# Kernel optimization log

Hardware: AMD Instinct MI355X
Metric: run time of the kernel (lower is better)

The kernel has to match this reference:

```python
import jax, jax.numpy as jnp
import numpy as np

HIDDEN = 1024
HEADS = 16
HEAD_DIM = HIDDEN // HEADS


def setup_inputs() -> dict:
    key = jax.random.key(0)
    ks = jax.random.split(key, 11)
    B, S = 2, 2048
    s = 1.0 / np.sqrt(HIDDEN)
    return {
        "query": jax.random.normal(ks[0], (B, S, HIDDEN), jnp.float32),
        "key": jax.random.normal(ks[1], (B, S, HIDDEN), jnp.float32),
        "value": jax.random.normal(ks[2], (B, S, HIDDEN), jnp.float32),
        "Wq": jax.random.uniform(ks[3], (HIDDEN, HIDDEN), jnp.float32, -s, s),
        "bq": jax.random.uniform(ks[4], (HIDDEN,), jnp.float32, -s, s),
        "Wk": jax.random.uniform(ks[5], (HIDDEN, HIDDEN), jnp.float32, -s, s),
        "bk": jax.random.uniform(ks[6], (HIDDEN,), jnp.float32, -s, s),
        "Wv": jax.random.uniform(ks[7], (HIDDEN, HIDDEN), jnp.float32, -s, s),
        "bv": jax.random.uniform(ks[8], (HIDDEN,), jnp.float32, -s, s),
        "Wo": jax.random.uniform(ks[9], (HIDDEN, HIDDEN), jnp.float32, -s, s),
        "bo": jax.random.uniform(ks[10], (HIDDEN,), jnp.float32, -s, s),
    }


def reference(query, key, value, Wq, bq, Wk, bk, Wv, bv, Wo, bo):
    B, Sq, _ = query.shape
    Sk = key.shape[1]
    # projections (torch Linear: x @ W^T + b)
    Q = (query @ Wq.T + bq).reshape(B, Sq, HEADS, HEAD_DIM).transpose(0, 2, 1, 3)
    K = (key @ Wk.T + bk).reshape(B, Sk, HEADS, HEAD_DIM).transpose(0, 2, 1, 3)
    V = (value @ Wv.T + bv).reshape(B, Sk, HEADS, HEAD_DIM).transpose(0, 2, 1, 3)
    scale = jnp.sqrt(jnp.float32(HEAD_DIM))
    scores = jnp.einsum("bhqd,bhkd->bhqk", Q, K) / scale  # [B,H,Sq,Sk]
    # causal mask (is_causal=True, Sq>1)
    causal = jnp.tril(jnp.ones((Sq, Sk), dtype=bool))
    scores = jnp.where(causal[None, None], scores, -jnp.inf)
    attn = jax.nn.softmax(scores, axis=-1)
    out = jnp.einsum("bhqk,bhkd->bhqd", attn, V)
    out = out.transpose(0, 2, 1, 3).reshape(B, Sq, HIDDEN)
    return out @ Wo.T + bo
```

## Files before the change

kernel.cpp:

```cpp
#include <hip/hip_runtime.h>
#include <hip/hip_bf16.h>


typedef __attribute__((ext_vector_type(4))) float f32x4;
typedef __attribute__((ext_vector_type(8))) short bf16x8;
typedef unsigned short u16;

#define SEQ   2048
#define NH    16
#define HD    64
#define HID   1024
#define CEXP  0.1803368801f
#define MEG   1048576u

#define BAR()  __builtin_amdgcn_s_barrier()
#define SCHED0() __builtin_amdgcn_sched_barrier(0)

static __device__ __forceinline__ u16 f2bf(float f) {
  union { __hip_bfloat16 h; u16 u; } c;
  c.h = __float2bfloat16(f);
  return c.u;
}

static __device__ __forceinline__ int swz(int row, int col8) {
  return col8 ^ ((row & 7) << 3);
}

static __device__ __forceinline__ void gll16(const void* g, void* l) {
  __builtin_amdgcn_global_load_lds(
      (const __attribute__((address_space(1))) void*)g,
      (__attribute__((address_space(3))) void*)l, 16, 0, 0);
}

__global__ __launch_bounds__(256) void cvt_kernel(
    const float* __restrict__ Wq, const float* __restrict__ Wk,
    const float* __restrict__ Wv, const float* __restrict__ Wo,
    const float* __restrict__ q, const float* __restrict__ k,
    const float* __restrict__ v,
    u16* __restrict__ wsout, u16* __restrict__ dob) {
  const int y = blockIdx.y;
  const int c = y & 3;
  const float* src;
  u16* dst;
  if (y < 4) {
    src = (y == 0) ? Wq : (y == 1) ? Wk : (y == 2) ? Wv : Wo;
    dst = wsout + (size_t)y * MEG;
  } else if (y < 8) {
    src = q + (size_t)c * MEG;
    dst = wsout + 4u * MEG + (size_t)c * MEG;
  } else if (y < 12) {
    src = k + (size_t)c * MEG;
    dst = dob + (size_t)c * MEG;
  } else {
    src = v + (size_t)c * MEG;
    dst = dob + 4u * MEG + (size_t)c * MEG;
  }
  int i = (blockIdx.x * 256 + threadIdx.x) * 4;
  float4 f = *(const float4*)(src + i);
  ushort4 o;
  o.x = f2bf(f.x); o.y = f2bf(f.y); o.z = f2bf(f.z); o.w = f2bf(f.w);
  *(ushort4*)(dst + i) = o;
}

__global__ __launch_bounds__(256) void proj_kernel(
    const u16* __restrict__ Xq, const u16* __restrict__ Xk,
    const u16* __restrict__ Xv, const u16* __restrict__ Wc,
    const float* __restrict__ bq, const float* __restrict__ bk,
    const float* __restrict__ bvp,
    u16* __restrict__ Qo, u16* __restrict__ Ko, u16* __restrict__ Vto) {
  __shared__ u16 As[2][128 * 64];
  __shared__ u16 Bs[2][128 * 64];

  const int tid  = threadIdx.x;
  const int lane = tid & 63;
  const int wid  = tid >> 6;
  const int wm   = wid >> 1, wn = wid & 1;
  const int l15  = lane & 15;
  const int lhi  = lane >> 4;
  const int z    = blockIdx.z;
  const int bm   = blockIdx.x * 128;
  const int bn   = blockIdx.y * 128;

  const u16* X = (z == 0) ? Xq : (z == 1) ? Xk : Xv;
  const u16* W = Wc + (size_t)z * (HID * HID);
  const float* bias = (z == 0) ? bq : (z == 1) ? bk : bvp;

  f32x4 acc[4][4];
#pragma unroll
  for (int i = 0; i < 4; i++)
#pragma unroll
    for (int j = 0; j < 4; j++) acc[i][j] = (f32x4){0.f, 0.f, 0.f, 0.f};

  const int lrow  = lane >> 3;
  const int gcol8 = lane & 7;

#define PROJ_STAGE(buf, k0)                                                       \
  {                                                                               \
    _Pragma("unroll")                                                             \
    for (int c = 0; c < 4; c++) {                                                 \
      const int row  = c * 32 + wid * 8 + lrow;                                   \
      const int scol = (gcol8 ^ (row & 7)) * 8;      \
      gll16(X + (size_t)(bm + row) * HID + (k0) + scol,                           \
            (char*)&As[buf][0] + c * 4096 + wid * 1024);                          \
      gll16(W + (size_t)(bn + row) * HID + (k0) + scol,                           \
            (char*)&Bs[buf][0] + c * 4096 + wid * 1024);                          \
    }                                                                             \
  }

  PROJ_STAGE(0, 0);
  for (int t = 0; t < 16; t++) {
    BAR();
    if (t < 15) {
      PROJ_STAGE((t + 1) & 1, (t + 1) * 64);
      asm volatile("s_waitcnt vmcnt(8)" ::: "memory");
    } else {
      asm volatile("s_waitcnt vmcnt(0)" ::: "memory");
    }
    BAR();
    SCHED0();
    const u16* A = &As[t & 1][0];
    const u16* B = &Bs[t & 1][0];
#pragma unroll
    for (int ks = 0; ks < 2; ks++) {
      bf16x8 af[4], bfm[4];
#pragma unroll
      for (int i = 0; i < 4; i++) {
        const int row = wm * 64 + i * 16 + l15;
        af[i] = *(const bf16x8*)&A[row * 64 + swz(row, ks * 32 + lhi * 8)];
      }
#pragma unroll
      for (int j = 0; j < 4; j++) {
        const int row = wn * 64 + j * 16 + l15;
        bfm[j] = *(const bf16x8*)&B[row * 64 + swz(row, ks * 32 + lhi * 8)];
      }
#pragma unroll
      for (int i = 0; i < 4; i++)
#pragma unroll
        for (int j = 0; j < 4; j++)
          acc[i][j] = __builtin_amdgcn_mfma_f32_16x16x32_bf16(af[i], bfm[j], acc[i][j], 0, 0, 0);
    }
  }
#undef PROJ_STAGE

  const int bb = bm >> 11;
#pragma unroll
  for (int j = 0; j < 4; j++) {
    const int n = bn + wn * 64 + j * 16 + l15;
    const float bv_ = bias[n];
    const int h = n >> 6, d = n & 63;
    if (z == 2) {
#pragma unroll
      for (int i = 0; i < 4; i++) {
        const int s0 = (bm + wm * 64 + i * 16 + lhi * 4) & 2047;
        ushort4 t;
        t.x = f2bf(acc[i][j][0] + bv_);
        t.y = f2bf(acc[i][j][1] + bv_);
        t.z = f2bf(acc[i][j][2] + bv_);
        t.w = f2bf(acc[i][j][3] + bv_);
        *(ushort4*)&Vto[((size_t)(bb * NH + h) * HD + d) * SEQ + s0] = t;
      }
    } else {
      u16* O = z ? Ko : Qo;
#pragma unroll
      for (int i = 0; i < 4; i++)
#pragma unroll
        for (int r = 0; r < 4; r++) {
          const int m = bm + wm * 64 + i * 16 + lhi * 4 + r;
          const int s = m & 2047;
          O[(((size_t)(bb * NH + h) * SEQ + s) << 6) + d] = f2bf(acc[i][j][r] + bv_);
        }
    }
  }
}

__global__ __launch_bounds__(512) void attn_kernel(
    const u16* __restrict__ Q, const u16* __restrict__ K,
    const u16* __restrict__ Vt, u16* __restrict__ Aout) {
  __shared__ __align__(16) char pool[34816];

  const int tid  = threadIdx.x;
  const int lane = tid & 63;
  const int wid  = tid >> 6;
  const int l15  = lane & 15;
  const int lhi  = lane >> 4;

  const int flat = blockIdx.x;
  const int slot = flat >> 3;
  const int bh   = (flat & 7) * 4 + (slot & 3);
  const int qt   = 15 - (slot >> 2);
  const int b    = bh >> 4, h = bh & 15;
  const size_t base = (size_t)bh * SEQ * HD;

  u16* Ksh = (u16*)(pool);
  u16* Vsh = (u16*)(pool + 8192);
  u16* Psh = (u16*)(pool + 16384 + wid * 2304);

  const int qrow = qt * 128 + wid * 16 + l15;
  bf16x8 aq[2];
  aq[0] = *(const bf16x8*)&Q[base + (size_t)qrow * HD + lhi * 8];
  aq[1] = *(const bf16x8*)&Q[base + (size_t)qrow * HD + 32 + lhi * 8];

  f32x4 o[4];
#pragma unroll
  for (int n = 0; n < 4; n++) o[n] = (f32x4){0.f, 0.f, 0.f, 0.f};
  float m_s = -1e30f, l_s = 0.f;

  const int srow = tid >> 3;
  const int sd   = (tid & 7) * 8;

  bf16x8 pk, pv;

#define ATTN_LOAD(kt_)                                                            \
  {                                                                               \
    pk = *(const bf16x8*)&K[base + (size_t)((kt_) * 64 + srow) * HD + sd];        \
    pv = *(const bf16x8*)&Vt[base + (size_t)srow * SEQ + (kt_) * 64 + sd];        \
  }

  ATTN_LOAD(0);

  const int nkt = 2 * qt + 2;
  for (int kt = 0; kt < nkt; ++kt) {
    BAR();
    *(bf16x8*)&Ksh[srow * 64 + swz(srow, sd)] = pk;
    *(bf16x8*)&Vsh[srow * 64 + swz(srow, sd)] = pv;
    if (kt + 1 < nkt) ATTN_LOAD(kt + 1);
    asm volatile("s_waitcnt lgkmcnt(0)" ::: "memory");
    BAR();
    SCHED0();
    {
      f32x4 sc[4];
      __builtin_amdgcn_s_setprio(1);
#pragma unroll
      for (int n = 0; n < 4; n++) {
        sc[n] = (f32x4){0.f, 0.f, 0.f, 0.f};
#pragma unroll
        for (int ks = 0; ks < 2; ks++) {
          const int krow = n * 16 + l15;
          bf16x8 bk = *(const bf16x8*)&Ksh[krow * 64 + swz(krow, ks * 32 + lhi * 8)];
          sc[n] = __builtin_amdgcn_mfma_f32_16x16x32_bf16(bk, aq[ks], sc[n], 0, 0, 0);
        }
      }
      __builtin_amdgcn_s_setprio(0);
      if (kt >= 2 * qt) {
#pragma unroll
        for (int n = 0; n < 4; n++)
#pragma unroll
          for (int r = 0; r < 4; r++)
            if (kt * 64 + n * 16 + lhi * 4 + r > qrow) sc[n][r] = -1e30f;
      }
      float mx = -1e30f;
#pragma unroll
      for (int n = 0; n < 4; n++)
        mx = fmaxf(mx, fmaxf(fmaxf(sc[n][0], sc[n][1]), fmaxf(sc[n][2], sc[n][3])));
      mx = fmaxf(mx, __shfl_xor(mx, 16, 64));
      mx = fmaxf(mx, __shfl_xor(mx, 32, 64));
      if (__any(mx > m_s + 64.0f)) {
        const float mnew = fmaxf(m_s, mx);
        const float fac = __builtin_amdgcn_exp2f((m_s - mnew) * CEXP);
        l_s *= fac;
        m_s = mnew;
        float facr[4];
#pragma unroll
        for (int r = 0; r < 4; r++) facr[r] = __shfl(fac, lhi * 4 + r, 64);
#pragma unroll
        for (int n = 0; n < 4; n++) {
          o[n][0] *= facr[0]; o[n][1] *= facr[1];
          o[n][2] *= facr[2]; o[n][3] *= facr[3];
        }
      }
      const float nmc = -m_s * CEXP;
      float ps = 0.f;
      u16 pb[4][4];
#pragma unroll
      for (int n = 0; n < 4; n++)
#pragma unroll
        for (int r = 0; r < 4; r++) {
          const float e = __builtin_amdgcn_exp2f(fmaf(sc[n][r], CEXP, nmc));
          ps += e;
          pb[n][r] = f2bf(e);
        }
      ps += __shfl_xor(ps, 16, 64);
      ps += __shfl_xor(ps, 32, 64);
      l_s += ps;
#pragma unroll
      for (int n = 0; n < 4; n++) {
        ushort4 t; t.x = pb[n][0]; t.y = pb[n][1]; t.z = pb[n][2]; t.w = pb[n][3];
        *(ushort4*)&Psh[l15 * 72 + n * 16 + lhi * 4] = t;
      }
      bf16x8 ap0 = *(const bf16x8*)&Psh[l15 * 72 + lhi * 8];
      bf16x8 ap1 = *(const bf16x8*)&Psh[l15 * 72 + 32 + lhi * 8];
      __builtin_amdgcn_s_setprio(1);
#pragma unroll
      for (int n = 0; n < 4; n++) {
        const int vrow = n * 16 + l15;
        bf16x8 bv0 = *(const bf16x8*)&Vsh[vrow * 64 + swz(vrow, lhi * 8)];
        bf16x8 bv1 = *(const bf16x8*)&Vsh[vrow * 64 + swz(vrow, 32 + lhi * 8)];
        o[n] = __builtin_amdgcn_mfma_f32_16x16x32_bf16(ap0, bv0, o[n], 0, 0, 0);
        o[n] = __builtin_amdgcn_mfma_f32_16x16x32_bf16(ap1, bv1, o[n], 0, 0, 0);
      }
      __builtin_amdgcn_s_setprio(0);
    }
  }
#undef ATTN_LOAD

  float l_o[4];
#pragma unroll
  for (int r = 0; r < 4; r++) l_o[r] = __shfl(l_s, lhi * 4 + r, 64);
#pragma unroll
  for (int n = 0; n < 4; n++) {
#pragma unroll
    for (int r = 0; r < 4; r++) {
      const int rowg = qt * 128 + wid * 16 + lhi * 4 + r;
      Aout[(((size_t)(b * SEQ + rowg)) << 10) + h * 64 + n * 16 + l15] =
          f2bf(o[n][r] / l_o[r]);
    }
  }
}

__global__ __launch_bounds__(256) void oproj_kernel(
    const u16* __restrict__ X, const u16* __restrict__ W,
    const float* __restrict__ bias, float* __restrict__ Out) {
  __shared__ u16 As[2][128 * 64];
  __shared__ u16 Bs[2][64 * 64];

  const int tid  = threadIdx.x;
  const int lane = tid & 63;
  const int wid  = tid >> 6;
  const int wm   = wid >> 1, wn = wid & 1;
  const int l15  = lane & 15;
  const int lhi  = lane >> 4;
  const int bm   = blockIdx.x * 128;
  const int bn   = blockIdx.y * 64;

  f32x4 acc[4][2];
#pragma unroll
  for (int i = 0; i < 4; i++)
#pragma unroll
    for (int j = 0; j < 2; j++) acc[i][j] = (f32x4){0.f, 0.f, 0.f, 0.f};

  const int lrow  = lane >> 3;
  const int gcol8 = lane & 7;

#define OPROJ_STAGE(buf, k0)                                                      \
  {                                                                               \
    _Pragma("unroll")                                                             \
    for (int c = 0; c < 4; c++) {                                                 \
      const int row  = c * 32 + wid * 8 + lrow;                                   \
      const int scol = (gcol8 ^ (row & 7)) * 8;                                   \
      gll16(X + (size_t)(bm + row) * HID + (k0) + scol,                           \
            (char*)&As[buf][0] + c * 4096 + wid * 1024);                          \
      if (c < 2)                                                                  \
        gll16(W + (size_t)(bn + row) * HID + (k0) + scol,                         \
              (char*)&Bs[buf][0] + c * 4096 + wid * 1024);                        \
    }                                                                             \
  }

  OPROJ_STAGE(0, 0);
  for (int t = 0; t < 16; t++) {
    BAR();
    if (t < 15) {
      OPROJ_STAGE((t + 1) & 1, (t + 1) * 64);
      asm volatile("s_waitcnt vmcnt(6)" ::: "memory");
    } else {
      asm volatile("s_waitcnt vmcnt(0)" ::: "memory");
    }
    BAR();
    SCHED0();
    const u16* A = &As[t & 1][0];
    const u16* B = &Bs[t & 1][0];
#pragma unroll
    for (int ks = 0; ks < 2; ks++) {
      bf16x8 af[4], bfm[2];
#pragma unroll
      for (int i = 0; i < 4; i++) {
        const int row = wm * 64 + i * 16 + l15;
        af[i] = *(const bf16x8*)&A[row * 64 + swz(row, ks * 32 + lhi * 8)];
      }
#pragma unroll
      for (int j = 0; j < 2; j++) {
        const int row = wn * 32 + j * 16 + l15;
        bfm[j] = *(const bf16x8*)&B[row * 64 + swz(row, ks * 32 + lhi * 8)];
      }
#pragma unroll
      for (int i = 0; i < 4; i++)
#pragma unroll
        for (int j = 0; j < 2; j++)
          acc[i][j] = __builtin_amdgcn_mfma_f32_16x16x32_bf16(af[i], bfm[j], acc[i][j], 0, 0, 0);
    }
  }
#undef OPROJ_STAGE

#pragma unroll
  for (int j = 0; j < 2; j++) {
    const int n = bn + wn * 32 + j * 16 + l15;
    const float bv_ = bias[n];
#pragma unroll
    for (int i = 0; i < 4; i++)
#pragma unroll
      for (int r = 0; r < 4; r++) {
        const int m = bm + wm * 64 + i * 16 + lhi * 4 + r;
        Out[(size_t)m * HID + n] = acc[i][j][r] + bv_;
      }
  }
}

extern "C" void kernel_launch(void* const* d_in, const int* in_sizes, int n_in,
                              void* d_out, int out_size, void* d_ws, size_t ws_size,
                              hipStream_t stream) {
  const float* q  = (const float*)d_in[0];
  const float* k  = (const float*)d_in[1];
  const float* v  = (const float*)d_in[2];
  const float* Wq = (const float*)d_in[3];
  const float* bq = (const float*)d_in[4];
  const float* Wk = (const float*)d_in[5];
  const float* bk = (const float*)d_in[6];
  const float* Wv = (const float*)d_in[7];
  const float* bv = (const float*)d_in[8];
  const float* Wo = (const float*)d_in[9];
  const float* bo = (const float*)d_in[10];

  u16* ws   = (u16*)d_ws;
  u16* wqkv = ws;
  u16* wob  = ws + 3u * MEG;
  u16* qb   = ws + 4u * MEG;
  u16* Qb   = ws + 8u * MEG;
  u16* Kb   = ws + 12u * MEG;
  u16* Vtb  = ws + 16u * MEG;
  u16* Ab   = qb;
  u16* kbf  = (u16*)d_out;
  u16* vbf  = (u16*)d_out + 4u * MEG;

  cvt_kernel<<<dim3(1024, 16), 256, 0, stream>>>(Wq, Wk, Wv, Wo, q, k, v, ws, kbf);

  proj_kernel<<<dim3(32, 8, 3), 256, 0, stream>>>(qb, kbf, vbf, wqkv, bq, bk, bv,
                                                  Qb, Kb, Vtb);

  attn_kernel<<<dim3(512), 512, 0, stream>>>(Qb, Kb, Vtb, Ab);

  oproj_kernel<<<dim3(32, 16), 256, 0, stream>>>(Ab, wob, bo, (float*)d_out);
}
```

Before: 115.3 us.

## Double-buffer K/V in LDS and compute next QK^T ahead of softmax

The attention loop now double-buffers K and V tiles in shared memory and software-pipelines the QK^T MFMA of the next key tile before the softmax and PV of the current tile. The aim is to let matrix-core work overlap the exp and reduction phase and to hide LDS-write and barrier latency. In exchange, shared memory grows from about 34 KB to 51 KB per block and an extra set of score registers is kept live, which may reduce occupancy or add register pressure.

```diff
diff --git a/kernel.cpp b/kernel.cpp
--- a/kernel.cpp
+++ b/kernel.cpp
@@ -176,7 +176,7 @@
 __global__ __launch_bounds__(512) void attn_kernel(
     const u16* __restrict__ Q, const u16* __restrict__ K,
     const u16* __restrict__ Vt, u16* __restrict__ Aout) {
-  __shared__ __align__(16) char pool[34816];
+  __shared__ __align__(16) char pool[51200];
 
   const int tid  = threadIdx.x;
   const int lane = tid & 63;
@@ -191,9 +191,7 @@
   const int b    = bh >> 4, h = bh & 15;
   const size_t base = (size_t)bh * SEQ * HD;
 
-  u16* Ksh = (u16*)(pool);
-  u16* Vsh = (u16*)(pool + 8192);
-  u16* Psh = (u16*)(pool + 16384 + wid * 2304);
+  u16* Psh = (u16*)(pool + 32768 + wid * 2304);
 
   const int qrow = qt * 128 + wid * 16 + l15;
   bf16x8 aq[2];
@@ -207,51 +205,71 @@
 
   const int srow = tid >> 3;
   const int sd   = (tid & 7) * 8;
+  const int swoff = srow * 64 + swz(srow, sd);
 
   bf16x8 pk, pv;
 
-#define ATTN_LOAD(kt_)                                                            \
+#define LOADR(kt_)                                                                \
   {                                                                               \
     pk = *(const bf16x8*)&K[base + (size_t)((kt_) * 64 + srow) * HD + sd];        \
     pv = *(const bf16x8*)&Vt[base + (size_t)srow * SEQ + (kt_) * 64 + sd];        \
   }
-
-  ATTN_LOAD(0);
+#define WRITE_LDS(b_)                                                             \
+  {                                                                               \
+    *(bf16x8*)&((u16*)(pool + (b_) * 8192))[swoff] = pk;                          \
+    *(bf16x8*)&((u16*)(pool + 16384 + (b_) * 8192))[swoff] = pv;                  \
+  }
+#define QKT(dst, b_, kt_)                                                         \
+  {                                                                               \
+    const u16* Ksh_ = (const u16*)(pool + (b_) * 8192);                           \
+    __builtin_amdgcn_s_setprio(1);                                                \
+    _Pragma("unroll")                                                             \
+    for (int n = 0; n < 4; n++) {                                                 \
+      dst[n] = (f32x4){0.f, 0.f, 0.f, 0.f};                                       \
+      _Pragma("unroll")                                                           \
+      for (int ks = 0; ks < 2; ks++) {                                            \
+        const int krow = n * 16 + l15;                                            \
+        bf16x8 bk = *(const bf16x8*)&Ksh_[krow * 64 + swz(krow, ks * 32 + lhi * 8)]; \
+        dst[n] = __builtin_amdgcn_mfma_f32_16x16x32_bf16(bk, aq[ks], dst[n], 0, 0, 0); \
+      }                                                                           \
+    }                                                                             \
+    __builtin_amdgcn_s_setprio(0);                                                \
+    if ((kt_) >= 2 * qt) {                                                        \
+      _Pragma("unroll")                                                           \
+      for (int n = 0; n < 4; n++)                                                 \
+        _Pragma("unroll")                                                         \
+        for (int r = 0; r < 4; r++)                                               \
+          if ((kt_) * 64 + n * 16 + lhi * 4 + r > qrow) dst[n][r] = -1e30f;       \
+    }                                                                             \
+  }
 
   const int nkt = 2 * qt + 2;
+
+  LOADR(0);
+  WRITE_LDS(0);
+  if (nkt > 1) LOADR(1);
+  asm volatile("s_waitcnt lgkmcnt(0)" ::: "memory");
+  BAR();
+  SCHED0();
+  f32x4 scc[4], scn[4];
+  QKT(scc, 0, 0);
+
   for (int kt = 0; kt < nkt; ++kt) {
-    BAR();
-    *(bf16x8*)&Ksh[srow * 64 + swz(srow, sd)] = pk;
-    *(bf16x8*)&Vsh[srow * 64 + swz(srow, sd)] = pv;
-    if (kt + 1 < nkt) ATTN_LOAD(kt + 1);
-    asm volatile("s_waitcnt lgkmcnt(0)" ::: "memory");
-    BAR();
-    SCHED0();
+    const int nk = kt + 1;
+    if (nk < nkt) {
+      BAR();
+      WRITE_LDS(nk & 1);
+      if (nk + 1 < nkt) LOADR(nk + 1);
+      asm volatile("s_waitcnt lgkmcnt(0)" ::: "memory");
+      BAR();
+      SCHED0();
+      QKT(scn, nk & 1, nk);
+    }
     {
-      f32x4 sc[4];
-      __builtin_amdgcn_s_setprio(1);
-#pragma unroll
-      for (int n = 0; n < 4; n++) {
-        sc[n] = (f32x4){0.f, 0.f, 0.f, 0.f};
-#pragma unroll
-        for (int ks = 0; ks < 2; ks++) {
-          const int krow = n * 16 + l15;
-          bf16x8 bk = *(const bf16x8*)&Ksh[krow * 64 + swz(krow, ks * 32 + lhi * 8)];
-          sc[n] = __builtin_amdgcn_mfma_f32_16x16x32_bf16(bk, aq[ks], sc[n], 0, 0, 0);
-        }
-      }
-      __builtin_amdgcn_s_setprio(0);
-      if (kt >= 2 * qt) {
-#pragma unroll
-        for (int n = 0; n < 4; n++)
-#pragma unroll
-          for (int r = 0; r < 4; r++)
-            if (kt * 64 + n * 16 + lhi * 4 + r > qrow) sc[n][r] = -1e30f;
-      }
       float mx = -1e30f;
 #pragma unroll
       for (int n = 0; n < 4; n++)
-        mx = fmaxf(mx, fmaxf(fmaxf(sc[n][0], sc[n][1]), fmaxf(sc[n][2], sc[n][3])));
+        mx = fmaxf(mx, fmaxf(fmaxf(scc[n][0], scc[n][1]), fmaxf(scc[n][2], scc[n][3])));
       mx = fmaxf(mx, __shfl_xor(mx, 16, 64));
       mx = fmaxf(mx, __shfl_xor(mx, 32, 64));
       if (__any(mx > m_s + 64.0f)) {
@@ -275,7 +293,7 @@
       for (int n = 0; n < 4; n++)
 #pragma unroll
         for (int r = 0; r < 4; r++) {
-          const float e = __builtin_amdgcn_exp2f(fmaf(sc[n][r], CEXP, nmc));
+          const float e = __builtin_amdgcn_exp2f(fmaf(scc[n][r], CEXP, nmc));
           ps += e;
           pb[n][r] = f2bf(e);
         }
@@ -289,6 +307,7 @@
       }
       bf16x8 ap0 = *(const bf16x8*)&Psh[l15 * 72 + lhi * 8];
       bf16x8 ap1 = *(const bf16x8*)&Psh[l15 * 72 + 32 + lhi * 8];
+      const u16* Vsh = (const u16*)(pool + 16384 + (kt & 1) * 8192);
       __builtin_amdgcn_s_setprio(1);
 #pragma unroll
       for (int n = 0; n < 4; n++) {
@@ -300,8 +319,12 @@
       }
       __builtin_amdgcn_s_setprio(0);
     }
-  }
-#undef ATTN_LOAD
+#pragma unroll
+    for (int n = 0; n < 4; n++) scc[n] = scn[n];
+  }
+#undef LOADR
+#undef WRITE_LDS
+#undef QKT
 
   float l_o[4];
 #pragma unroll
```

After: 115.8 us. No clear change (+0.4%).

## Rewrite attention kernel with 32x32x16 MFMA and register-resident P

Applied to the files above, without the earlier changes.

The attention kernel moves from 16x16x32 to 32x32x16 bf16 MFMA tiles. Each of 4 waves now owns 32 query rows, so blocks shrink to 256 threads with a launch bound of 4 blocks per CU. The K and V tiles use new swizzled LDS layouts matched to the 32x32 operand pattern. Because the score accumulator layout matches the A-operand layout, the softmax probabilities are packed to bf16 in registers and fed directly to the PV MFMA, removing the per-wave P round trip through LDS. The cost is higher register pressure from the f32x16 accumulators and fewer waves per block to hide latency.

```diff
diff --git a/kernel.cpp b/kernel.cpp
--- a/kernel.cpp
+++ b/kernel.cpp
@@ -2,8 +2,9 @@
 #include <hip/hip_bf16.h>
 
 
-typedef __attribute__((ext_vector_type(4))) float f32x4;
-typedef __attribute__((ext_vector_type(8))) short bf16x8;
+typedef __attribute__((ext_vector_type(4)))  float f32x4;
+typedef __attribute__((ext_vector_type(16))) float f32x16;
+typedef __attribute__((ext_vector_type(8)))  short bf16x8;
 typedef unsigned short u16;
 
 #define SEQ   2048
@@ -13,7 +14,7 @@
 #define CEXP  0.1803368801f
 #define MEG   1048576u
 
-#define BAR()  __builtin_amdgcn_s_barrier()
+#define BAR()    __builtin_amdgcn_s_barrier()
 #define SCHED0() __builtin_amdgcn_sched_barrier(0)
 
 static __device__ __forceinline__ u16 f2bf(float f) {
@@ -99,7 +100,7 @@
     _Pragma("unroll")                                                             \
     for (int c = 0; c < 4; c++) {                                                 \
       const int row  = c * 32 + wid * 8 + lrow;                                   \
-      const int scol = (gcol8 ^ (row & 7)) * 8;      \
+      const int scol = (gcol8 ^ (row & 7)) * 8;                                   \
       gll16(X + (size_t)(bm + row) * HID + (k0) + scol,                           \
             (char*)&As[buf][0] + c * 4096 + wid * 1024);                          \
       gll16(W + (size_t)(bn + row) * HID + (k0) + scol,                           \
@@ -173,16 +174,18 @@
   }
 }
 
-__global__ __launch_bounds__(512) void attn_kernel(
+__global__ __launch_bounds__(256, 4) void attn_kernel(
     const u16* __restrict__ Q, const u16* __restrict__ K,
     const u16* __restrict__ Vt, u16* __restrict__ Aout) {
-  __shared__ __align__(16) char pool[34816];
+  __shared__ __align__(16) char pool[16384];
+  u16* Ksh = (u16*)pool;
+  u16* Vsh = (u16*)(pool + 8192);
 
   const int tid  = threadIdx.x;
   const int lane = tid & 63;
   const int wid  = tid >> 6;
-  const int l15  = lane & 15;
-  const int lhi  = lane >> 4;
+  const int l31  = lane & 31;
+  const int g    = lane >> 5;
 
   const int flat = blockIdx.x;
   const int slot = flat >> 3;
@@ -191,130 +194,149 @@
   const int b    = bh >> 4, h = bh & 15;
   const size_t base = (size_t)bh * SEQ * HD;
 
-  u16* Ksh = (u16*)(pool);
-  u16* Vsh = (u16*)(pool + 8192);
-  u16* Psh = (u16*)(pool + 16384 + wid * 2304);
-
-  const int qrow = qt * 128 + wid * 16 + l15;
-  bf16x8 aq[2];
-  aq[0] = *(const bf16x8*)&Q[base + (size_t)qrow * HD + lhi * 8];
-  aq[1] = *(const bf16x8*)&Q[base + (size_t)qrow * HD + 32 + lhi * 8];
-
-  f32x4 o[4];
-#pragma unroll
-  for (int n = 0; n < 4; n++) o[n] = (f32x4){0.f, 0.f, 0.f, 0.f};
+  const int qrow = qt * 128 + wid * 32 + l31;
+  bf16x8 aq[4];
+#pragma unroll
+  for (int ds = 0; ds < 4; ds++)
+    aq[ds] = *(const bf16x8*)&Q[base + (size_t)qrow * HD + ds * 16 + g * 8];
+
+  f32x16 o[2];
+#pragma unroll
+  for (int r = 0; r < 16; r++) { o[0][r] = 0.f; o[1][r] = 0.f; }
   float m_s = -1e30f, l_s = 0.f;
 
-  const int srow = tid >> 3;
-  const int sd   = (tid & 7) * 8;
-
-  bf16x8 pk, pv;
-
-#define ATTN_LOAD(kt_)                                                            \
+  const int srow = tid >> 2;
+  const int sd   = (tid & 3) * 16;
+  const int krow = srow & 31;
+  const int kcb  = ((srow >> 5) * 64 + sd) >> 3;
+  u16* kdst0 = &Ksh[krow * 128 + (((kcb)     ^ (krow & 15)) << 3)];
+  u16* kdst1 = &Ksh[krow * 128 + (((kcb + 1) ^ (krow & 15)) << 3)];
+  const int vg0 = sd >> 2;
+
+  union B2S { bf16x8 v; short4 s[2]; };
+  B2S pk0, pk1, pv0, pv1;
+
+#define LOADR(kt_)                                                                \
   {                                                                               \
-    pk = *(const bf16x8*)&K[base + (size_t)((kt_) * 64 + srow) * HD + sd];        \
-    pv = *(const bf16x8*)&Vt[base + (size_t)srow * SEQ + (kt_) * 64 + sd];        \
-  }
-
-  ATTN_LOAD(0);
+    const u16* kp = K + base + (size_t)((kt_) * 64 + srow) * HD + sd;             \
+    pk0.v = *(const bf16x8*)kp;                                                   \
+    pk1.v = *(const bf16x8*)(kp + 8);                                             \
+    const u16* vp = Vt + base + (size_t)srow * SEQ + (kt_) * 64 + sd;             \
+    pv0.v = *(const bf16x8*)vp;                                                   \
+    pv1.v = *(const bf16x8*)(vp + 8);                                             \
+  }
+
+  LOADR(0);
 
   const int nkt = 2 * qt + 2;
   for (int kt = 0; kt < nkt; ++kt) {
     BAR();
-    *(bf16x8*)&Ksh[srow * 64 + swz(srow, sd)] = pk;
-    *(bf16x8*)&Vsh[srow * 64 + swz(srow, sd)] = pv;
-    if (kt + 1 < nkt) ATTN_LOAD(kt + 1);
+    *(bf16x8*)kdst0 = pk0.v;
+    *(bf16x8*)kdst1 = pk1.v;
+#pragma unroll
+    for (int i = 0; i < 4; i++) {
+      short4 hv = (i < 2) ? pv0.s[i & 1] : pv1.s[i & 1];
+      *(short4*)&Vsh[srow * 64 + (((vg0 + i) ^ (srow & 15)) << 2)] = hv;
+    }
+    if (kt + 1 < nkt) LOADR(kt + 1);
     asm volatile("s_waitcnt lgkmcnt(0)" ::: "memory");
     BAR();
     SCHED0();
-    {
-      f32x4 sc[4];
-      __builtin_amdgcn_s_setprio(1);
-#pragma unroll
-      for (int n = 0; n < 4; n++) {
-        sc[n] = (f32x4){0.f, 0.f, 0.f, 0.f};
-#pragma unroll
-        for (int ks = 0; ks < 2; ks++) {
-          const int krow = n * 16 + l15;
-          bf16x8 bk = *(const bf16x8*)&Ksh[krow * 64 + swz(krow, ks * 32 + lhi * 8)];
-          sc[n] = __builtin_amdgcn_mfma_f32_16x16x32_bf16(bk, aq[ks], sc[n], 0, 0, 0);
+
+    f32x16 sc[2];
+    __builtin_amdgcn_s_setprio(1);
+#pragma unroll
+    for (int kb = 0; kb < 2; kb++) {
+#pragma unroll
+      for (int r = 0; r < 16; r++) sc[kb][r] = 0.f;
+#pragma unroll
+      for (int ds = 0; ds < 4; ds++) {
+        const int cc = kb * 8 + ds * 2 + g;
+        bf16x8 kf = *(const bf16x8*)&Ksh[l31 * 128 + ((cc ^ (l31 & 15)) << 3)];
+        sc[kb] = __builtin_amdgcn_mfma_f32_32x32x16_bf16(kf, aq[ds], sc[kb], 0, 0, 0);
+      }
+    }
+    __builtin_amdgcn_s_setprio(0);
+
+    if (kt >= 2 * qt) {
+#pragma unroll
+      for (int kb = 0; kb < 2; kb++)
+#pragma unroll
+        for (int r = 0; r < 16; r++) {
+          const int kg = kt * 64 + kb * 32 + (r & 3) + 8 * (r >> 2) + 4 * g;
+          if (kg > qrow) sc[kb][r] = -1e30f;
         }
-      }
-      __builtin_amdgcn_s_setprio(0);
-      if (kt >= 2 * qt) {
-#pragma unroll
-        for (int n = 0; n < 4; n++)
-#pragma unroll
-          for (int r = 0; r < 4; r++)
-            if (kt * 64 + n * 16 + lhi * 4 + r > qrow) sc[n][r] = -1e30f;
-      }
-      float mx = -1e30f;
-#pragma unroll
-      for (int n = 0; n < 4; n++)
-        mx = fmaxf(mx, fmaxf(fmaxf(sc[n][0], sc[n][1]), fmaxf(sc[n][2], sc[n][3])));
-      mx = fmaxf(mx, __shfl_xor(mx, 16, 64));
-      mx = fmaxf(mx, __shfl_xor(mx, 32, 64));
-      if (__any(mx > m_s + 64.0f)) {
-        const float mnew = fmaxf(m_s, mx);
-        const float fac = __builtin_amdgcn_exp2f((m_s - mnew) * CEXP);
-        l_s *= fac;
-        m_s = mnew;
-        float facr[4];
-#pragma unroll
-        for (int r = 0; r < 4; r++) facr[r] = __shfl(fac, lhi * 4 + r, 64);
-#pragma unroll
-        for (int n = 0; n < 4; n++) {
-          o[n][0] *= facr[0]; o[n][1] *= facr[1];
-          o[n][2] *= facr[2]; o[n][3] *= facr[3];
-        }
-      }
-      const float nmc = -m_s * CEXP;
-      float ps = 0.f;
-      u16 pb[4][4];
-#pragma unroll
-      for (int n = 0; n < 4; n++)
-#pragma unroll
-        for (int r = 0; r < 4; r++) {
-          const float e = __builtin_amdgcn_exp2f(fmaf(sc[n][r], CEXP, nmc));
-          ps += e;
-          pb[n][r] = f2bf(e);
-        }
-      ps += __shfl_xor(ps, 16, 64);
-      ps += __shfl_xor(ps, 32, 64);
-      l_s += ps;
-#pragma unroll
-      for (int n = 0; n < 4; n++) {
-        ushort4 t; t.x = pb[n][0]; t.y = pb[n][1]; t.z = pb[n][2]; t.w = pb[n][3];
-        *(ushort4*)&Psh[l15 * 72 + n * 16 + lhi * 4] = t;
-      }
-      bf16x8 ap0 = *(const bf16x8*)&Psh[l15 * 72 + lhi * 8];
-      bf16x8 ap1 = *(const bf16x8*)&Psh[l15 * 72 + 32 + lhi * 8];
-      __builtin_amdgcn_s_setprio(1);
-#pragma unroll
-      for (int n = 0; n < 4; n++) {
-        const int vrow = n * 16 + l15;
-        bf16x8 bv0 = *(const bf16x8*)&Vsh[vrow * 64 + swz(vrow, lhi * 8)];
-        bf16x8 bv1 = *(const bf16x8*)&Vsh[vrow * 64 + swz(vrow, 32 + lhi * 8)];
-        o[n] = __builtin_amdgcn_mfma_f32_16x16x32_bf16(ap0, bv0, o[n], 0, 0, 0);
-        o[n] = __builtin_amdgcn_mfma_f32_16x16x32_bf16(ap1, bv1, o[n], 0, 0, 0);
-      }
-      __builtin_amdgcn_s_setprio(0);
-    }
-  }
-#undef ATTN_LOAD
-
-  float l_o[4];
-#pragma unroll
-  for (int r = 0; r < 4; r++) l_o[r] = __shfl(l_s, lhi * 4 + r, 64);
-#pragma unroll
-  for (int n = 0; n < 4; n++) {
-#pragma unroll
-    for (int r = 0; r < 4; r++) {
-      const int rowg = qt * 128 + wid * 16 + lhi * 4 + r;
-      Aout[(((size_t)(b * SEQ + rowg)) << 10) + h * 64 + n * 16 + l15] =
-          f2bf(o[n][r] / l_o[r]);
-    }
-  }
+    }
+
+    float mx = -1e30f;
+#pragma unroll
+    for (int kb = 0; kb < 2; kb++)
+#pragma unroll
+      for (int r = 0; r < 16; r++) mx = fmaxf(mx, sc[kb][r]);
+    mx = fmaxf(mx, __shfl_xor(mx, 32, 64));
+    if (__any(mx > m_s + 64.0f)) {
+      const float mnew = fmaxf(m_s, mx);
+      const float fac = __builtin_amdgcn_exp2f((m_s - mnew) * CEXP);
+      l_s *= fac;
+      m_s = mnew;
+#pragma unroll
+      for (int r = 0; r < 16; r++) {
+        const float fr = __shfl(fac, (r & 3) + 8 * (r >> 2) + 4 * g, 64);
+        o[0][r] *= fr;
+        o[1][r] *= fr;
+      }
+    }
+    const float nmc = -m_s * CEXP;
+    float ps = 0.f;
+#pragma unroll
+    for (int kb = 0; kb < 2; kb++)
+#pragma unroll
+      for (int r = 0; r < 16; r++) {
+        const float e = __builtin_amdgcn_exp2f(fmaf(sc[kb][r], CEXP, nmc));
+        sc[kb][r] = e;
+        ps += e;
+      }
+    ps += __shfl_xor(ps, 32, 64);
+    l_s += ps;
+
+    __builtin_amdgcn_s_setprio(1);
+#pragma unroll
+    for (int s = 0; s < 4; s++) {
+      const int kb = s >> 1, rb = (s & 1) * 8;
+      bf16x8 pa;
+#pragma unroll
+      for (int j = 0; j < 8; j++) pa[j] = (short)f2bf(sc[kb][rb + j]);
+#pragma unroll
+      for (int dt = 0; dt < 2; dt++) {
+        const int row = dt * 32 + l31;
+        const int ga = ((4 * s + g)     ^ (row & 15)) << 2;
+        const int gb = ((4 * s + g + 2) ^ (row & 15)) << 2;
+        short4 b0 = *(const short4*)&Vsh[row * 64 + ga];
+        short4 b1 = *(const short4*)&Vsh[row * 64 + gb];
+        bf16x8 bv;
+        bv[0] = b0.x; bv[1] = b0.y; bv[2] = b0.z; bv[3] = b0.w;
+        bv[4] = b1.x; bv[5] = b1.y; bv[6] = b1.z; bv[7] = b1.w;
+        o[dt] = __builtin_amdgcn_mfma_f32_32x32x16_bf16(pa, bv, o[dt], 0, 0, 0);
+      }
+    }
+    __builtin_amdgcn_s_setprio(0);
+  }
+#undef LOADR
+
+  float inv[16];
+#pragma unroll
+  for (int r = 0; r < 16; r++) {
+    const float lr = __shfl(l_s, (r & 3) + 8 * (r >> 2) + 4 * g, 64);
+    inv[r] = 1.0f / lr;
+  }
+#pragma unroll
+  for (int dt = 0; dt < 2; dt++)
+#pragma unroll
+    for (int r = 0; r < 16; r++) {
+      const int rowg = qt * 128 + wid * 32 + (r & 3) + 8 * (r >> 2) + 4 * g;
+      Aout[(((size_t)(b * SEQ + rowg)) << 10) + h * 64 + dt * 32 + l31] =
+          f2bf(o[dt][r] * inv[r]);
+    }
 }
 
 __global__ __launch_bounds__(256) void oproj_kernel(
@@ -435,7 +457,7 @@
   proj_kernel<<<dim3(32, 8, 3), 256, 0, stream>>>(qb, kbf, vbf, wqkv, bq, bk, bv,
                                                   Qb, Kb, Vtb);
 
-  attn_kernel<<<dim3(512), 512, 0, stream>>>(Qb, Kb, Vtb, Ab);
+  attn_kernel<<<dim3(512), 256, 0, stream>>>(Qb, Kb, Vtb, Ab);
 
   oproj_kernel<<<dim3(32, 16), 256, 0, stream>>>(Ab, wob, bo, (float*)d_out);
 }
```

Result: slower. 152.7 us (+32.5%).
